# Performance work log

Hardware: AMD Instinct MI355X
Metric: run time of the kernel (lower is better)

The kernel has to match this reference:

```python
import jax, jax.numpy as jnp
import numpy as np

N_POINTS = 524288
N_VOXELS = 32768
C_IN = 6
GF = 64          # gf_dim
C_OUT = 256      # output_channels
HALF = C_OUT // 2


def _linear_params(key, fin, fout):
    kw, kb = jax.random.split(key)
    bound = 1.0 / np.sqrt(fin)
    W = jax.random.uniform(kw, (fin, fout), jnp.float32, -bound, bound)
    b = jax.random.uniform(kb, (fout,), jnp.float32, -bound, bound)
    return W, b


def setup_inputs() -> dict:
    key = jax.random.key(0)
    ks = jax.random.split(key, 8)
    inp_feat = jax.random.normal(ks[0], (N_POINTS, C_IN), dtype=jnp.float32)
    vox2point_idx = jax.random.randint(ks[1], (N_POINTS,), 0, N_VOXELS, dtype=jnp.int64)
    W1, b1 = _linear_params(ks[2], C_IN, GF)          # point_lin1
    W2, b2 = _linear_params(ks[3], GF, HALF)          # point_lin2
    Wv1, bv1 = _linear_params(ks[4], HALF, HALF)      # vox_lin1
    W3, b3 = _linear_params(ks[5], C_OUT, C_OUT)      # point_lin3
    W4, b4 = _linear_params(ks[6], C_OUT, C_OUT)      # point_lin4
    Wv2, bv2 = _linear_params(ks[7], C_OUT, C_OUT)    # vox_lin2
    return {
        "inp_feat": inp_feat, "vox2point_idx": vox2point_idx, "num_voxels": N_VOXELS,
        "W1": W1, "b1": b1, "W2": W2, "b2": b2, "Wv1": Wv1, "bv1": bv1,
        "W3": W3, "b3": b3, "W4": W4, "b4": b4, "Wv2": Wv2, "bv2": bv2,
    }


def reference(inp_feat, vox2point_idx, num_voxels,
              W1, b1, W2, b2, Wv1, bv1, W3, b3, W4, b4, Wv2, bv2):
    relu = jax.nn.relu
    # per-point MLP: [N,6] -> [N,64] -> [N,128]
    point_feat1 = relu(inp_feat @ W1 + b1)
    point_feat2 = relu(point_feat1 @ W2 + b2)
    # scatter-max pooling over voxels: [N,128] -> [V,128]
    occ_voxel_feat = jax.ops.segment_max(point_feat2, vox2point_idx,
                                         num_segments=num_voxels)
    occ_voxel_feat = relu(occ_voxel_feat @ Wv1 + bv1)
    # gather voxel feature back to points and concat: [N,128]+[N,128] -> [N,256]
    point_global_feat = occ_voxel_feat[vox2point_idx]
    point_feat3 = jnp.concatenate((point_global_feat, point_feat2), axis=-1)
    point_feat4 = relu(point_feat3 @ W3 + b3)
    point_feat5 = relu(point_feat4 @ W4 + b4)
    # second scatter-max pooling: [N,256] -> [V,256]
    occ_voxel_feat2 = jax.ops.segment_max(point_feat5, vox2point_idx,
                                          num_segments=num_voxels)
    occ_voxel_feat2 = relu(occ_voxel_feat2 @ Wv2 + bv2)
    return occ_voxel_feat2
```

## Files before the change

### kernel.cpp

```cpp
#include <hip/hip_runtime.h>


#define NPTS 524288
#define NVOX 32768

typedef _Float16 f16;
typedef _Float16 f16x8 __attribute__((ext_vector_type(8)));
typedef float f32x4 __attribute__((ext_vector_type(4)));

#define GLDS16(g, l)                                                          \
  __builtin_amdgcn_global_load_lds(                                           \
      (const __attribute__((address_space(1))) unsigned int*)(const void*)(g),\
      (__attribute__((address_space(3))) unsigned int*)(void*)(l), 16, 0, 0)

__global__ void k_fixidx(const int* __restrict__ raw, int* __restrict__ out) {
  bool is64 = true;
#pragma unroll
  for (int k = 0; k < 32; ++k)
    if (raw[2 * k + 1] != 0) is64 = false;
  int stride = gridDim.x * blockDim.x;
  for (int i = blockIdx.x * blockDim.x + threadIdx.x; i < NPTS; i += stride)
    out[i] = is64 ? raw[2 * i] : raw[i];
}

__global__ void k_hist(const int* __restrict__ idx, int* __restrict__ counts) {
  int stride = gridDim.x * blockDim.x;
  for (int i = blockIdx.x * blockDim.x + threadIdx.x; i < NPTS; i += stride)
    atomicAdd(&counts[idx[i]], 1);
}

__global__ void k_scan(const int* __restrict__ counts, int* __restrict__ offsets) {
  __shared__ int part[1024];
  __shared__ int sums[32];
  int t = threadIdx.x;
  int loc[32];
  int s = 0;
#pragma unroll
  for (int j = 0; j < 32; ++j) { loc[j] = counts[t * 32 + j]; s += loc[j]; }
  part[t] = s;
  __syncthreads();
  if (t < 32) {
    int run = 0;
    for (int j = 0; j < 32; ++j) { int tmp = part[t * 32 + j]; part[t * 32 + j] = run; run += tmp; }
    sums[t] = run;
  }
  __syncthreads();
  if (t == 0) {
    int run = 0;
    for (int i = 0; i < 32; ++i) { int tmp = sums[i]; sums[i] = run; run += tmp; }
  }
  __syncthreads();
  int b = part[t] + sums[t >> 5];
#pragma unroll
  for (int j = 0; j < 32; ++j) { offsets[t * 32 + j] = b; b += loc[j]; }
  if (t == 1023) offsets[NVOX] = b;
}

__global__ void k_scat(const int* __restrict__ idx, const int* __restrict__ offsets,
                       int* __restrict__ cursor, int* __restrict__ sp, int* __restrict__ sv) {
  int stride = gridDim.x * blockDim.x;
  for (int i = blockIdx.x * blockDim.x + threadIdx.x; i < NPTS; i += stride) {
    int v = idx[i];
    int pos = offsets[v] + atomicAdd(&cursor[v], 1);
    sp[pos] = i;
    sv[pos] = v;
  }
}

__global__ void k_wcast(const float* __restrict__ W, f16* __restrict__ Wt, int K, int N) {
  int g = blockIdx.x * blockDim.x + threadIdx.x;
  if (g >= K * N) return;
  int k = g / N, n = g % N;
  Wt[n * K + k] = (f16)W[g];
}

__global__ void k_castf(const float* __restrict__ in, f16* __restrict__ out, int n) {
  int stride = gridDim.x * blockDim.x;
  for (int i = blockIdx.x * blockDim.x + threadIdx.x; i < n; i += stride)
    out[i] = (f16)in[i];
}

template <int K, int N, int MODEA, bool SCATTER, bool OUTF32, bool WRITEO, bool WTILE>
__global__ __launch_bounds__(256, 3) void k_gemm(
    const f16* __restrict__ A,
    const int* __restrict__ sv, const int* __restrict__ sp,
    const int* __restrict__ offs,
    const float* __restrict__ x, const float* __restrict__ W1, const float* __restrict__ b1,
    const f16* __restrict__ Bt,
    const float* __restrict__ bias,
    f16* __restrict__ Of16, float* __restrict__ Of32, int row0) {
  constexpr int NT = N / 128;
  __shared__ __align__(16) char smem[32768];
  __shared__ float xs[MODEA == 2 ? 768 : 1];
  __shared__ int svp[MODEA == 2 ? 128 : 1];
  __shared__ int svx[SCATTER ? 128 : 1];
  f16* As = (f16*)smem;
  f16* Bs = As + 128 * 64;

  int nwg = gridDim.x;
  int bid = blockIdx.x;
  int q = nwg >> 3;
  int swz = (bid & 7) * q + (bid >> 3);
  int tm = swz / NT, tn = swz % NT;
  int t = threadIdx.x;

  if (MODEA == 2) { if (t < 128) svp[t] = sp[row0 + tm * 128 + t]; }
  if (SCATTER) { if (t < 128) svx[t] = sv[row0 + tm * 128 + t]; }
  if (MODEA == 2) __syncthreads();

  int l = t & 63, w = t >> 6;
  int wm = w >> 1, wn = w & 1;
  int lrow = l & 15, lk = l >> 4;
  f32x4 acc[4][4] = {};

  constexpr int KT = K / 64;
#pragma unroll
  for (int kt = 0; kt < KT; ++kt) {
    int k0 = kt * 64;
#pragma unroll
    for (int i = 0; i < 4; ++i) {
      int n = i * 32 + (t >> 3);
      int clog = (t & 7) ^ (n & 7);
      GLDS16(Bt + (size_t)(tn * 128 + n) * K + k0 + clog * 8, Bs + i * 2048 + t * 8);
    }
    if constexpr (MODEA == 2) {
      for (int g = t; g < 768; g += 256) xs[g] = x[(size_t)svp[g / 6] * 6 + (g % 6)];
      __syncthreads();
      int j = t & 63;
      float wv[6];
#pragma unroll
      for (int i = 0; i < 6; ++i) wv[i] = W1[i * 64 + j];
      float bb = b1[j];
      int rb = (t >> 6) * 32;
#pragma unroll
      for (int rr = 0; rr < 32; ++rr) {
        int row = rb + rr;
        float a = bb;
#pragma unroll
        for (int i = 0; i < 6; ++i) a += xs[row * 6 + i] * wv[i];
        As[row * 64 + (((j >> 3) ^ (row & 7)) << 3) + (j & 7)] = (f16)fmaxf(a, 0.f);
      }
    } else {
#pragma unroll
      for (int i = 0; i < 4; ++i) {
        int row = i * 32 + (t >> 3);
        int clog = (t & 7) ^ (row & 7);
        GLDS16(A + (size_t)(tm * 128 + row) * K + k0 + clog * 8, As + i * 2048 + t * 8);
      }
    }
    __syncthreads();
#pragma unroll
    for (int ks = 0; ks < 2; ++ks) {
      f16x8 af[4], bf[4];
#pragma unroll
      for (int m = 0; m < 4; ++m) {
        int row = wm * 64 + m * 16 + lrow;
        int cp = (ks * 4 + lk) ^ (row & 7);
        af[m] = *(const f16x8*)(As + row * 64 + cp * 8);
      }
#pragma unroll
      for (int n = 0; n < 4; ++n) {
        int col = wn * 64 + n * 16 + lrow;
        int cp = (ks * 4 + lk) ^ (col & 7);
        bf[n] = *(const f16x8*)(Bs + col * 64 + cp * 8);
      }
#pragma unroll
      for (int m = 0; m < 4; ++m)
#pragma unroll
        for (int n = 0; n < 4; ++n)
          acc[m][n] = __builtin_amdgcn_mfma_f32_16x16x32_f16(af[m], bf[n], acc[m][n], 0, 0, 0);
    }
    __syncthreads();
  }

  if constexpr (WRITEO) {
#pragma unroll
    for (int m = 0; m < 4; ++m)
#pragma unroll
      for (int n = 0; n < 4; ++n)
#pragma unroll
        for (int j = 0; j < 4; ++j) {
          int row = wm * 64 + m * 16 + lk * 4 + j;
          int gc  = tn * 128 + wn * 64 + n * 16 + lrow;
          float val = fmaxf(acc[m][n][j] + bias[gc], 0.f);
          if constexpr (OUTF32) Of32[(size_t)(tm * 128 + row) * N + gc] = val;
          else                  Of16[(size_t)(tm * 128 + row) * N + gc] = (f16)val;
        }
  }

  if constexpr (SCATTER) {
    f16* tile = (f16*)smem;
#pragma unroll
    for (int m = 0; m < 4; ++m)
#pragma unroll
      for (int n = 0; n < 4; ++n)
#pragma unroll
        for (int j = 0; j < 4; ++j) {
          int row = wm * 64 + m * 16 + lk * 4 + j;
          int col = wn * 64 + n * 16 + lrow;
          tile[row * 128 + col] =
              (f16)fmaxf(acc[m][n][j] + bias[tn * 128 + col], 0.f);
        }
    __syncthreads();
    if constexpr (WTILE) {
      f16* dst = Of16 + (size_t)(row0 + tm * 128) * 128;
#pragma unroll
      for (int i = 0; i < 8; ++i) {
        int g = i * 256 + t;
        *(f16x8*)(dst + g * 8) = *(const f16x8*)(tile + g * 8);
      }
    }
    int c = t & 127, h = t >> 7;
    int r0l = h * 64;
    int gc = tn * 128 + c;
    int grow0 = row0 + tm * 128 + r0l;
    float run = 0.f;
    int curv = svx[r0l];
    for (int r = r0l; r < r0l + 64; ++r) {
      int v = svx[r];
      if (v != curv) {
        bool inter = (offs[curv] >= grow0) && (offs[curv + 1] <= grow0 + 64);
        if (inter) Of32[(size_t)curv * N + gc] = run;
        else atomicMax((int*)&Of32[(size_t)curv * N + gc], __float_as_int(run));
        curv = v; run = 0.f;
      }
      run = fmaxf(run, (float)tile[r * 128 + c]);
    }
    bool inter = (offs[curv] >= grow0) && (offs[curv + 1] <= grow0 + 64);
    if (inter) Of32[(size_t)curv * N + gc] = run;
    else atomicMax((int*)&Of32[(size_t)curv * N + gc], __float_as_int(run));
  }
}

__global__ __launch_bounds__(512, 2) void k_stage2(
    const f16* __restrict__ pf2, const f16* __restrict__ occ1,
    const int* __restrict__ sv, const int* __restrict__ offs,
    const f16* __restrict__ W3t, const float* __restrict__ b3,
    const f16* __restrict__ W4t, const float* __restrict__ b4,
    float* __restrict__ vox2f, int row0) {
  __shared__ __align__(16) f16 Bs[256 * 32];
  __shared__ __align__(16) f16 PF[64 * 264];
  __shared__ int svx[64];

  int nwg = gridDim.x;
  int bid = blockIdx.x;
  int q = nwg >> 3;
  int bm = (bid & 7) * q + (bid >> 3);
  int t = threadIdx.x;
  int l = t & 63, w = t >> 6;
  int lrow = l & 15, lk = l >> 4;

  if (t < 64) svx[t] = sv[row0 + bm * 64 + t];
  __syncthreads();

  f16* Afull = PF;
#pragma unroll
  for (int ii = 0; ii < 4; ++ii) {
    int g = ii * 512 + t;
    int row = g >> 5, cs = g & 31;
    int cl = (cs & 24) | ((cs ^ row) & 7);
    const f16* src;
    if (cl < 16) src = occ1 + (size_t)svx[row] * 128 + cl * 8;
    else         src = pf2 + (size_t)(bm * 64 + row) * 128 + (cl - 16) * 8;
    GLDS16(src, Afull + g * 8);
  }
#pragma unroll
  for (int ii = 0; ii < 2; ++ii) {
    int g = ii * 512 + t;
    int n = g >> 2, c = g & 3;
    int cl = c ^ ((n >> 1) & 3);
    GLDS16(W3t + (size_t)n * 256 + cl * 8, Bs + g * 8);
  }
  __syncthreads();

  f32x4 acc[4][2] = {};

#pragma unroll
  for (int p = 0; p < 8; ++p) {
    f16x8 bf[2];
#pragma unroll
    for (int n = 0; n < 2; ++n) {
      int col = w * 32 + n * 16 + lrow;
      int cp = lk ^ ((col >> 1) & 3);
      bf[n] = *(const f16x8*)(Bs + col * 32 + cp * 8);
    }
    __syncthreads();
    {
      const f16* Wsrc = (p < 7) ? W3t : W4t;
      int kc = (p < 7) ? (p + 1) : 0;
#pragma unroll
      for (int ii = 0; ii < 2; ++ii) {
        int g = ii * 512 + t;
        int n = g >> 2, c = g & 3;
        int cl = c ^ ((n >> 1) & 3);
        GLDS16(Wsrc + (size_t)n * 256 + kc * 32 + cl * 8, Bs + g * 8);
      }
    }
    __builtin_amdgcn_s_setprio(1);
    f16x8 af[4];
#pragma unroll
    for (int m = 0; m < 4; ++m) {
      int row = m * 16 + lrow;
      int ab = p * 4 + lk;
      int slot = (ab & 24) | ((ab ^ row) & 7);
      af[m] = *(const f16x8*)(Afull + row * 256 + slot * 8);
    }
#pragma unroll
    for (int m = 0; m < 4; ++m)
#pragma unroll
      for (int n = 0; n < 2; ++n)
        acc[m][n] = __builtin_amdgcn_mfma_f32_16x16x32_f16(af[m], bf[n], acc[m][n], 0, 0, 0);
    __builtin_amdgcn_s_setprio(0);
    __syncthreads();
  }

  f16* pf4 = PF;
#pragma unroll
  for (int m = 0; m < 4; ++m)
#pragma unroll
    for (int n = 0; n < 2; ++n)
#pragma unroll
      for (int j = 0; j < 4; ++j) {
        int row  = m * 16 + lk * 4 + j;
        int colg = w * 32 + n * 16 + lrow;
        pf4[row * 264 + colg] = (f16)fmaxf(acc[m][n][j] + b3[colg], 0.f);
      }
  __syncthreads();

#pragma unroll
  for (int m = 0; m < 4; ++m)
#pragma unroll
    for (int n = 0; n < 2; ++n)
      acc[m][n] = (f32x4){0.f, 0.f, 0.f, 0.f};

#pragma unroll
  for (int p = 0; p < 8; ++p) {
    f16x8 bf[2];
#pragma unroll
    for (int n = 0; n < 2; ++n) {
      int col = w * 32 + n * 16 + lrow;
      int cp = lk ^ ((col >> 1) & 3);
      bf[n] = *(const f16x8*)(Bs + col * 32 + cp * 8);
    }
    __syncthreads();
    if (p < 7) {
#pragma unroll
      for (int ii = 0; ii < 2; ++ii) {
        int g = ii * 512 + t;
        int n = g >> 2, c = g & 3;
        int cl = c ^ ((n >> 1) & 3);
        GLDS16(W4t + (size_t)n * 256 + (p + 1) * 32 + cl * 8, Bs + g * 8);
      }
    }
    __builtin_amdgcn_s_setprio(1);
    f16x8 af[4];
#pragma unroll
    for (int m = 0; m < 4; ++m) {
      int row = m * 16 + lrow;
      int chunk = p * 4 + lk;
      af[m] = *(const f16x8*)(pf4 + row * 264 + chunk * 8);
    }
#pragma unroll
    for (int m = 0; m < 4; ++m)
#pragma unroll
      for (int n = 0; n < 2; ++n)
        acc[m][n] = __builtin_amdgcn_mfma_f32_16x16x32_f16(af[m], bf[n], acc[m][n], 0, 0, 0);
    __builtin_amdgcn_s_setprio(0);
    __syncthreads();
  }

  f16* pf5 = PF;
#pragma unroll
  for (int m = 0; m < 4; ++m)
#pragma unroll
    for (int n = 0; n < 2; ++n)
#pragma unroll
      for (int j = 0; j < 4; ++j) {
        int row  = m * 16 + lk * 4 + j;
        int colg = w * 32 + n * 16 + lrow;
        pf5[row * 264 + colg] = (f16)fmaxf(acc[m][n][j] + b4[colg], 0.f);
      }
  __syncthreads();

  {
    int c = t & 255, seg = t >> 8;
    int r0l = seg * 32;
    int grow0 = row0 + bm * 64 + r0l;
    float run = 0.f;
    int curv = svx[r0l];
    for (int r = r0l; r < r0l + 32; ++r) {
      int v = svx[r];
      if (v != curv) {
        bool inter = (offs[curv] >= grow0) && (offs[curv + 1] <= grow0 + 32);
        if (inter) vox2f[(size_t)curv * 256 + c] = run;
        else atomicMax((int*)&vox2f[(size_t)curv * 256 + c], __float_as_int(run));
        curv = v; run = 0.f;
      }
      run = fmaxf(run, (float)pf5[r * 264 + c]);
    }
    bool inter = (offs[curv] >= grow0) && (offs[curv + 1] <= grow0 + 32);
    if (inter) vox2f[(size_t)curv * 256 + c] = run;
    else atomicMax((int*)&vox2f[(size_t)curv * 256 + c], __float_as_int(run));
  }
}

extern "C" void kernel_launch(void* const* d_in, const int* in_sizes, int n_in,
                              void* d_out, int out_size, void* d_ws, size_t ws_size,
                              hipStream_t stream) {
  const float* x   = (const float*)d_in[0];
  const int*  idxr = (const int*)d_in[1];
  const float* W1  = (const float*)d_in[3];
  const float* b1  = (const float*)d_in[4];
  const float* W2  = (const float*)d_in[5];
  const float* b2  = (const float*)d_in[6];
  const float* Wv1 = (const float*)d_in[7];
  const float* bv1 = (const float*)d_in[8];
  const float* W3  = (const float*)d_in[9];
  const float* b3  = (const float*)d_in[10];
  const float* W4  = (const float*)d_in[11];
  const float* b4  = (const float*)d_in[12];
  const float* Wv2 = (const float*)d_in[13];
  const float* bv2 = (const float*)d_in[14];
  float* out = (float*)d_out;

  char* ws = (char*)d_ws;
  size_t off = 0;
  auto alloc = [&](size_t bytes) {
    void* p = ws + off;
    off = (off + bytes + 255) & ~(size_t)255;
    return p;
  };
  int* idx     = (int*)alloc((size_t)NPTS * 4);
  int* counts  = (int*)alloc((size_t)NVOX * 4);
  int* cursor  = (int*)alloc((size_t)NVOX * 4);
  int* offs    = (int*)alloc((size_t)(NVOX + 1) * 4);
  int* sp      = (int*)alloc((size_t)NPTS * 4);
  int* sv      = (int*)alloc((size_t)NPTS * 4);
  f16* W2t     = (f16*)alloc(64 * 128 * 2);
  f16* Wv1t    = (f16*)alloc(128 * 128 * 2);
  f16* W3t     = (f16*)alloc(256 * 256 * 2);
  f16* W4t     = (f16*)alloc(256 * 256 * 2);
  f16* Wv2t    = (f16*)alloc(256 * 256 * 2);
  float* vox1f = (float*)alloc((size_t)NVOX * 128 * 4);
  f16* vox1h   = (f16*)alloc((size_t)NVOX * 128 * 2);
  f16* occ1    = (f16*)alloc((size_t)NVOX * 128 * 2);
  float* vox2f = (float*)alloc((size_t)NVOX * 256 * 4);

  size_t rem = (ws_size > off) ? ws_size - off : 0;
  bool PF2FULL = rem >= (size_t)NPTS * 256 + 4096;
  int CH = 65536;
  f16* pf2   = (f16*)alloc(PF2FULL ? (size_t)NPTS * 256 : (size_t)CH * 256);
  f16* vox2h = pf2;

  hipMemsetAsync(counts, 0, (size_t)NVOX * 4, stream);
  hipMemsetAsync(cursor, 0, (size_t)NVOX * 4, stream);
  hipMemsetAsync(vox1f, 0, (size_t)NVOX * 128 * 4, stream);
  hipMemsetAsync(vox2f, 0, (size_t)NVOX * 256 * 4, stream);

  k_fixidx<<<2048, 256, 0, stream>>>(idxr, idx);
  k_wcast<<<(64 * 128 + 255) / 256, 256, 0, stream>>>(W2, W2t, 64, 128);
  k_wcast<<<(128 * 128 + 255) / 256, 256, 0, stream>>>(Wv1, Wv1t, 128, 128);
  k_wcast<<<(256 * 256 + 255) / 256, 256, 0, stream>>>(W3, W3t, 256, 256);
  k_wcast<<<(256 * 256 + 255) / 256, 256, 0, stream>>>(W4, W4t, 256, 256);
  k_wcast<<<(256 * 256 + 255) / 256, 256, 0, stream>>>(Wv2, Wv2t, 256, 256);
  k_hist<<<2048, 256, 0, stream>>>(idx, counts);
  k_scan<<<1, 1024, 0, stream>>>(counts, offs);
  k_scat<<<2048, 256, 0, stream>>>(idx, offs, cursor, sp, sv);

  if (PF2FULL)
    k_gemm<64, 128, 2, true, false, false, true><<<NPTS / 128, 256, 0, stream>>>(
        nullptr, sv, sp, offs, x, W1, b1, W2t, b2, pf2, vox1f, 0);
  else
    k_gemm<64, 128, 2, true, false, false, false><<<NPTS / 128, 256, 0, stream>>>(
        nullptr, sv, sp, offs, x, W1, b1, W2t, b2, nullptr, vox1f, 0);
  k_castf<<<2048, 256, 0, stream>>>(vox1f, vox1h, NVOX * 128);
  k_gemm<128, 128, 0, false, false, true, false><<<NVOX / 128, 256, 0, stream>>>(
      vox1h, nullptr, nullptr, nullptr, nullptr, nullptr, nullptr,
      Wv1t, bv1, occ1, nullptr, 0);

  if (PF2FULL) {
    k_stage2<<<NPTS / 64, 512, 0, stream>>>(
        pf2, occ1, sv, offs, W3t, b3, W4t, b4, vox2f, 0);
  } else {
    for (int c = 0; c < NPTS / CH; ++c) {
      int row0 = c * CH;
      k_gemm<64, 128, 2, false, false, true, false><<<CH / 128, 256, 0, stream>>>(
          nullptr, nullptr, sp, nullptr, x, W1, b1, W2t, b2, pf2, nullptr, row0);
      k_stage2<<<CH / 64, 512, 0, stream>>>(
          pf2, occ1, sv, offs, W3t, b3, W4t, b4, vox2f, row0);
    }
  }

  k_castf<<<2048, 256, 0, stream>>>(vox2f, vox2h, NVOX * 256);
  k_gemm<256, 256, 0, false, true, true, false><<<(NVOX / 128) * 2, 256, 0, stream>>>(
      vox2h, nullptr, nullptr, nullptr, nullptr, nullptr, nullptr,
      Wv2t, bv2, nullptr, out, 0);
}
```

Before: 387.0 us.

## Precompute voxel half of point_lin3 per voxel instead of per point

Splits W3 into a voxel half and a point half. The voxel half (occ1 @ W3top + b3) is computed once per voxel by a new GEMM into a voxc buffer. k_stage2 then gathers that precomputed partial sum into its accumulators and runs only the K=128 point half. This removes half of the per-point layer-3 matmul FLOPs. In exchange it adds a small extra GEMM, a 32768x256 f16 intermediate, scalar per-element gathers of voxc into registers, and XOR swizzling of the pf4/pf5 LDS tiles.

```diff
diff --git a/kernel.cpp b/kernel.cpp
--- a/kernel.cpp
+++ b/kernel.cpp
@@ -74,13 +74,20 @@
   Wt[n * K + k] = (f16)W[g];
 }
 
+__global__ void k_wcast2(const float* __restrict__ W, f16* __restrict__ Wt, int k0) {
+  int g = blockIdx.x * blockDim.x + threadIdx.x;
+  if (g >= 256 * 128) return;
+  int n = g >> 7, k = g & 127;
+  Wt[g] = (f16)W[(size_t)(k0 + k) * 256 + n];
+}
+
 __global__ void k_castf(const float* __restrict__ in, f16* __restrict__ out, int n) {
   int stride = gridDim.x * blockDim.x;
   for (int i = blockIdx.x * blockDim.x + threadIdx.x; i < n; i += stride)
     out[i] = (f16)in[i];
 }
 
-template <int K, int N, int MODEA, bool SCATTER, bool OUTF32, bool WRITEO, bool WTILE>
+template <int K, int N, int MODEA, bool SCATTER, bool OUTF32, bool WRITEO, bool WTILE, bool RELU>
 __global__ __launch_bounds__(256, 3) void k_gemm(
     const f16* __restrict__ A,
     const int* __restrict__ sv, const int* __restrict__ sp,
@@ -182,7 +189,8 @@
         for (int j = 0; j < 4; ++j) {
           int row = wm * 64 + m * 16 + lk * 4 + j;
           int gc  = tn * 128 + wn * 64 + n * 16 + lrow;
-          float val = fmaxf(acc[m][n][j] + bias[gc], 0.f);
+          float val = acc[m][n][j] + bias[gc];
+          if constexpr (RELU) val = fmaxf(val, 0.f);
           if constexpr (OUTF32) Of32[(size_t)(tm * 128 + row) * N + gc] = val;
           else                  Of16[(size_t)(tm * 128 + row) * N + gc] = (f16)val;
         }
@@ -233,14 +241,18 @@
 }
 
 __global__ __launch_bounds__(512, 2) void k_stage2(
-    const f16* __restrict__ pf2, const f16* __restrict__ occ1,
+    const f16* __restrict__ pf2, const f16* __restrict__ voxc,
     const int* __restrict__ sv, const int* __restrict__ offs,
-    const f16* __restrict__ W3t, const float* __restrict__ b3,
-    const f16* __restrict__ W4t, const float* __restrict__ b4,
+    const f16* __restrict__ W3bt,
+    const f16* __restrict__ W4t,
+    const float* __restrict__ b4,
     float* __restrict__ vox2f, int row0) {
-  __shared__ __align__(16) f16 Bs[256 * 32];
-  __shared__ __align__(16) f16 PF[64 * 264];
+  __shared__ __align__(16) char smem[49152];
   __shared__ int svx[64];
+  f16* As  = (f16*)smem;
+  f16* Bs  = (f16*)(smem + 32768);
+  f16* pf4 = (f16*)smem;
+  f16* pf5 = pf4;
 
   int nwg = gridDim.x;
   int bid = blockIdx.x;
@@ -253,30 +265,34 @@
   if (t < 64) svx[t] = sv[row0 + bm * 64 + t];
   __syncthreads();
 
-  f16* Afull = PF;
-#pragma unroll
-  for (int ii = 0; ii < 4; ++ii) {
+#pragma unroll
+  for (int ii = 0; ii < 2; ++ii) {
     int g = ii * 512 + t;
-    int row = g >> 5, cs = g & 31;
-    int cl = (cs & 24) | ((cs ^ row) & 7);
-    const f16* src;
-    if (cl < 16) src = occ1 + (size_t)svx[row] * 128 + cl * 8;
-    else         src = pf2 + (size_t)(bm * 64 + row) * 128 + (cl - 16) * 8;
-    GLDS16(src, Afull + g * 8);
+    int row = g >> 4, cs = g & 15;
+    int cl = (cs & 8) | ((cs ^ row) & 7);
+    GLDS16(pf2 + (size_t)(bm * 64 + row) * 128 + cl * 8, As + g * 8);
   }
 #pragma unroll
   for (int ii = 0; ii < 2; ++ii) {
     int g = ii * 512 + t;
     int n = g >> 2, c = g & 3;
     int cl = c ^ ((n >> 1) & 3);
-    GLDS16(W3t + (size_t)n * 256 + cl * 8, Bs + g * 8);
-  }
-  __syncthreads();
-
-  f32x4 acc[4][2] = {};
-
-#pragma unroll
-  for (int p = 0; p < 8; ++p) {
+    GLDS16(W3bt + (size_t)n * 128 + cl * 8, Bs + g * 8);
+  }
+  f32x4 acc[4][2];
+#pragma unroll
+  for (int m = 0; m < 4; ++m)
+#pragma unroll
+    for (int j = 0; j < 4; ++j) {
+      int v = svx[m * 16 + lk * 4 + j];
+#pragma unroll
+      for (int n = 0; n < 2; ++n)
+        acc[m][n][j] = (float)voxc[(size_t)v * 256 + w * 32 + n * 16 + lrow];
+    }
+  __syncthreads();
+
+#pragma unroll
+  for (int p = 0; p < 4; ++p) {
     f16x8 bf[2];
 #pragma unroll
     for (int n = 0; n < 2; ++n) {
@@ -285,15 +301,21 @@
       bf[n] = *(const f16x8*)(Bs + col * 32 + cp * 8);
     }
     __syncthreads();
-    {
-      const f16* Wsrc = (p < 7) ? W3t : W4t;
-      int kc = (p < 7) ? (p + 1) : 0;
+    if (p < 3) {
 #pragma unroll
       for (int ii = 0; ii < 2; ++ii) {
         int g = ii * 512 + t;
         int n = g >> 2, c = g & 3;
         int cl = c ^ ((n >> 1) & 3);
-        GLDS16(Wsrc + (size_t)n * 256 + kc * 32 + cl * 8, Bs + g * 8);
+        GLDS16(W3bt + (size_t)n * 128 + (p + 1) * 32 + cl * 8, Bs + g * 8);
+      }
+    } else {
+#pragma unroll
+      for (int ii = 0; ii < 2; ++ii) {
+        int g = ii * 512 + t;
+        int n = g >> 2, c = g & 3;
+        int cl = c ^ ((n >> 1) & 3);
+        GLDS16(W4t + (size_t)n * 256 + cl * 8, Bs + g * 8);
       }
     }
     __builtin_amdgcn_s_setprio(1);
@@ -302,8 +324,8 @@
     for (int m = 0; m < 4; ++m) {
       int row = m * 16 + lrow;
       int ab = p * 4 + lk;
-      int slot = (ab & 24) | ((ab ^ row) & 7);
-      af[m] = *(const f16x8*)(Afull + row * 256 + slot * 8);
+      int slot = (ab & 8) | ((ab ^ row) & 7);
+      af[m] = *(const f16x8*)(As + row * 128 + slot * 8);
     }
 #pragma unroll
     for (int m = 0; m < 4; ++m)
@@ -314,7 +336,6 @@
     __syncthreads();
   }
 
-  f16* pf4 = PF;
 #pragma unroll
   for (int m = 0; m < 4; ++m)
 #pragma unroll
@@ -323,7 +344,9 @@
       for (int j = 0; j < 4; ++j) {
         int row  = m * 16 + lk * 4 + j;
         int colg = w * 32 + n * 16 + lrow;
-        pf4[row * 264 + colg] = (f16)fmaxf(acc[m][n][j] + b3[colg], 0.f);
+        int ch = colg >> 3;
+        int sc = (ch & 24) | ((ch ^ row) & 7);
+        pf4[row * 256 + sc * 8 + (colg & 7)] = (f16)fmaxf(acc[m][n][j], 0.f);
       }
   __syncthreads();
 
@@ -358,7 +381,8 @@
     for (int m = 0; m < 4; ++m) {
       int row = m * 16 + lrow;
       int chunk = p * 4 + lk;
-      af[m] = *(const f16x8*)(pf4 + row * 264 + chunk * 8);
+      int slot = (chunk & 24) | ((chunk ^ row) & 7);
+      af[m] = *(const f16x8*)(pf4 + row * 256 + slot * 8);
     }
 #pragma unroll
     for (int m = 0; m < 4; ++m)
@@ -369,7 +393,6 @@
     __syncthreads();
   }
 
-  f16* pf5 = PF;
 #pragma unroll
   for (int m = 0; m < 4; ++m)
 #pragma unroll
@@ -378,7 +401,9 @@
       for (int j = 0; j < 4; ++j) {
         int row  = m * 16 + lk * 4 + j;
         int colg = w * 32 + n * 16 + lrow;
-        pf5[row * 264 + colg] = (f16)fmaxf(acc[m][n][j] + b4[colg], 0.f);
+        int ch = colg >> 3;
+        int sc = (ch & 24) | ((ch ^ row) & 7);
+        pf5[row * 256 + sc * 8 + (colg & 7)] = (f16)fmaxf(acc[m][n][j] + b4[colg], 0.f);
       }
   __syncthreads();
 
@@ -388,6 +413,7 @@
     int grow0 = row0 + bm * 64 + r0l;
     float run = 0.f;
     int curv = svx[r0l];
+    int ch = c >> 3;
     for (int r = r0l; r < r0l + 32; ++r) {
       int v = svx[r];
       if (v != curv) {
@@ -396,7 +422,8 @@
         else atomicMax((int*)&vox2f[(size_t)curv * 256 + c], __float_as_int(run));
         curv = v; run = 0.f;
       }
-      run = fmaxf(run, (float)pf5[r * 264 + c]);
+      int sc = (ch & 24) | ((ch ^ r) & 7);
+      run = fmaxf(run, (float)pf5[r * 256 + sc * 8 + (c & 7)]);
     }
     bool inter = (offs[curv] >= grow0) && (offs[curv + 1] <= grow0 + 32);
     if (inter) vox2f[(size_t)curv * 256 + c] = run;
@@ -438,12 +465,14 @@
   int* sv      = (int*)alloc((size_t)NPTS * 4);
   f16* W2t     = (f16*)alloc(64 * 128 * 2);
   f16* Wv1t    = (f16*)alloc(128 * 128 * 2);
-  f16* W3t     = (f16*)alloc(256 * 256 * 2);
+  f16* W3topt  = (f16*)alloc(256 * 128 * 2);
+  f16* W3bott  = (f16*)alloc(256 * 128 * 2);
   f16* W4t     = (f16*)alloc(256 * 256 * 2);
   f16* Wv2t    = (f16*)alloc(256 * 256 * 2);
   float* vox1f = (float*)alloc((size_t)NVOX * 128 * 4);
   f16* vox1h   = (f16*)alloc((size_t)NVOX * 128 * 2);
   f16* occ1    = (f16*)alloc((size_t)NVOX * 128 * 2);
+  f16* voxc    = (f16*)alloc((size_t)NVOX * 256 * 2);
   float* vox2f = (float*)alloc((size_t)NVOX * 256 * 4);
 
   size_t rem = (ws_size > off) ? ws_size - off : 0;
@@ -460,7 +489,8 @@
   k_fixidx<<<2048, 256, 0, stream>>>(idxr, idx);
   k_wcast<<<(64 * 128 + 255) / 256, 256, 0, stream>>>(W2, W2t, 64, 128);
   k_wcast<<<(128 * 128 + 255) / 256, 256, 0, stream>>>(Wv1, Wv1t, 128, 128);
-  k_wcast<<<(256 * 256 + 255) / 256, 256, 0, stream>>>(W3, W3t, 256, 256);
+  k_wcast2<<<(256 * 128 + 255) / 256, 256, 0, stream>>>(W3, W3topt, 0);
+  k_wcast2<<<(256 * 128 + 255) / 256, 256, 0, stream>>>(W3, W3bott, 128);
   k_wcast<<<(256 * 256 + 255) / 256, 256, 0, stream>>>(W4, W4t, 256, 256);
   k_wcast<<<(256 * 256 + 255) / 256, 256, 0, stream>>>(Wv2, Wv2t, 256, 256);
   k_hist<<<2048, 256, 0, stream>>>(idx, counts);
@@ -468,31 +498,34 @@
   k_scat<<<2048, 256, 0, stream>>>(idx, offs, cursor, sp, sv);
 
   if (PF2FULL)
-    k_gemm<64, 128, 2, true, false, false, true><<<NPTS / 128, 256, 0, stream>>>(
+    k_gemm<64, 128, 2, true, false, false, true, true><<<NPTS / 128, 256, 0, stream>>>(
         nullptr, sv, sp, offs, x, W1, b1, W2t, b2, pf2, vox1f, 0);
   else
-    k_gemm<64, 128, 2, true, false, false, false><<<NPTS / 128, 256, 0, stream>>>(
+    k_gemm<64, 128, 2, true, false, false, false, true><<<NPTS / 128, 256, 0, stream>>>(
         nullptr, sv, sp, offs, x, W1, b1, W2t, b2, nullptr, vox1f, 0);
   k_castf<<<2048, 256, 0, stream>>>(vox1f, vox1h, NVOX * 128);
-  k_gemm<128, 128, 0, false, false, true, false><<<NVOX / 128, 256, 0, stream>>>(
+  k_gemm<128, 128, 0, false, false, true, false, true><<<NVOX / 128, 256, 0, stream>>>(
       vox1h, nullptr, nullptr, nullptr, nullptr, nullptr, nullptr,
       Wv1t, bv1, occ1, nullptr, 0);
+  k_gemm<128, 256, 0, false, false, true, false, false><<<(NVOX / 128) * 2, 256, 0, stream>>>(
+      occ1, nullptr, nullptr, nullptr, nullptr, nullptr, nullptr,
+      W3topt, b3, voxc, nullptr, 0);
 
   if (PF2FULL) {
     k_stage2<<<NPTS / 64, 512, 0, stream>>>(
-        pf2, occ1, sv, offs, W3t, b3, W4t, b4, vox2f, 0);
+        pf2, voxc, sv, offs, W3bott, W4t, b4, vox2f, 0);
   } else {
     for (int c = 0; c < NPTS / CH; ++c) {
       int row0 = c * CH;
-      k_gemm<64, 128, 2, false, false, true, false><<<CH / 128, 256, 0, stream>>>(
+      k_gemm<64, 128, 2, false, false, true, false, true><<<CH / 128, 256, 0, stream>>>(
           nullptr, nullptr, sp, nullptr, x, W1, b1, W2t, b2, pf2, nullptr, row0);
       k_stage2<<<CH / 64, 512, 0, stream>>>(
-          pf2, occ1, sv, offs, W3t, b3, W4t, b4, vox2f, row0);
+          pf2, voxc, sv, offs, W3bott, W4t, b4, vox2f, row0);
     }
   }
 
   k_castf<<<2048, 256, 0, stream>>>(vox2f, vox2h, NVOX * 256);
-  k_gemm<256, 256, 0, false, true, true, false><<<(NVOX / 128) * 2, 256, 0, stream>>>(
+  k_gemm<256, 256, 0, false, true, true, false, true><<<(NVOX / 128) * 2, 256, 0, stream>>>(
       vox2h, nullptr, nullptr, nullptr, nullptr, nullptr, nullptr,
       Wv2t, bv2, nullptr, out, 0);
 }
```

Result: slower. 430.7 us (+11.3%).

## Split first MLP layer into standalone kernel and XOR-swizzle stage2 LDS tile

Applied to the files above, without the earlier changes.

Adds a k_mlp1 kernel that computes the 6->64 layer in sorted point order and writes an f16 intermediate buffer. When workspace allows, the first GEMM then reads it in MODEA 0 instead of recomputing the layer inline. Separately, the stage2 shared tile drops its 264-element row padding in favour of an XOR swizzle on 8-element chunks, which shrinks LDS use while aiming to keep reads conflict-free. The split costs an extra NPTS*64 f16 write and read through global memory plus one more launch.

```diff
diff --git a/kernel.cpp b/kernel.cpp
--- a/kernel.cpp
+++ b/kernel.cpp
@@ -64,6 +64,39 @@
     int pos = offsets[v] + atomicAdd(&cursor[v], 1);
     sp[pos] = i;
     sv[pos] = v;
+  }
+}
+
+__global__ void k_mlp1(const float* __restrict__ x, const int* __restrict__ sp,
+                       const float* __restrict__ W1, const float* __restrict__ b1,
+                       f16* __restrict__ pf1) {
+  __shared__ float w[384];
+  __shared__ float bb[64];
+  int t = threadIdx.x;
+  if (t < 384) w[t] = W1[t];
+  if (t < 64) bb[t] = b1[t];
+  __syncthreads();
+  int stride = gridDim.x * blockDim.x;
+  for (int s = blockIdx.x * blockDim.x + t; s < NPTS; s += stride) {
+    int p = sp[s];
+    const float* src = x + (size_t)p * 6;
+    float x0 = src[0], x1 = src[1], x2 = src[2];
+    float x3 = src[3], x4 = src[4], x5 = src[5];
+    f16* dst = pf1 + (size_t)s * 64;
+#pragma unroll
+    for (int j0 = 0; j0 < 64; j0 += 8) {
+      f16x8 o;
+#pragma unroll
+      for (int u = 0; u < 8; ++u) {
+        int j = j0 + u;
+        float a = bb[j];
+        a += x0 * w[j];       a += x1 * w[64 + j];
+        a += x2 * w[128 + j]; a += x3 * w[192 + j];
+        a += x4 * w[256 + j]; a += x5 * w[320 + j];
+        o[u] = (f16)fmaxf(a, 0.f);
+      }
+      *(f16x8*)(dst + j0) = o;
+    }
   }
 }
 
@@ -239,7 +272,7 @@
     const f16* __restrict__ W4t, const float* __restrict__ b4,
     float* __restrict__ vox2f, int row0) {
   __shared__ __align__(16) f16 Bs[256 * 32];
-  __shared__ __align__(16) f16 PF[64 * 264];
+  __shared__ __align__(16) f16 PF[64 * 256];
   __shared__ int svx[64];
 
   int nwg = gridDim.x;
@@ -323,7 +356,9 @@
       for (int j = 0; j < 4; ++j) {
         int row  = m * 16 + lk * 4 + j;
         int colg = w * 32 + n * 16 + lrow;
-        pf4[row * 264 + colg] = (f16)fmaxf(acc[m][n][j] + b3[colg], 0.f);
+        int ch = colg >> 3;
+        int sc = (ch & 24) | ((ch ^ row) & 7);
+        pf4[row * 256 + sc * 8 + (colg & 7)] = (f16)fmaxf(acc[m][n][j] + b3[colg], 0.f);
       }
   __syncthreads();
 
@@ -358,7 +393,8 @@
     for (int m = 0; m < 4; ++m) {
       int row = m * 16 + lrow;
       int chunk = p * 4 + lk;
-      af[m] = *(const f16x8*)(pf4 + row * 264 + chunk * 8);
+      int slot = (chunk & 24) | ((chunk ^ row) & 7);
+      af[m] = *(const f16x8*)(pf4 + row * 256 + slot * 8);
     }
 #pragma unroll
     for (int m = 0; m < 4; ++m)
@@ -378,7 +414,9 @@
       for (int j = 0; j < 4; ++j) {
         int row  = m * 16 + lk * 4 + j;
         int colg = w * 32 + n * 16 + lrow;
-        pf5[row * 264 + colg] = (f16)fmaxf(acc[m][n][j] + b4[colg], 0.f);
+        int ch = colg >> 3;
+        int sc = (ch & 24) | ((ch ^ row) & 7);
+        pf5[row * 256 + sc * 8 + (colg & 7)] = (f16)fmaxf(acc[m][n][j] + b4[colg], 0.f);
       }
   __syncthreads();
 
@@ -388,6 +426,7 @@
     int grow0 = row0 + bm * 64 + r0l;
     float run = 0.f;
     int curv = svx[r0l];
+    int ch = c >> 3;
     for (int r = r0l; r < r0l + 32; ++r) {
       int v = svx[r];
       if (v != curv) {
@@ -396,7 +435,8 @@
         else atomicMax((int*)&vox2f[(size_t)curv * 256 + c], __float_as_int(run));
         curv = v; run = 0.f;
       }
-      run = fmaxf(run, (float)pf5[r * 264 + c]);
+      int sc = (ch & 24) | ((ch ^ r) & 7);
+      run = fmaxf(run, (float)pf5[r * 256 + sc * 8 + (c & 7)]);
     }
     bool inter = (offs[curv] >= grow0) && (offs[curv + 1] <= grow0 + 32);
     if (inter) vox2f[(size_t)curv * 256 + c] = run;
@@ -451,6 +491,9 @@
   int CH = 65536;
   f16* pf2   = (f16*)alloc(PF2FULL ? (size_t)NPTS * 256 : (size_t)CH * 256);
   f16* vox2h = pf2;
+  size_t rem2 = (ws_size > off) ? ws_size - off : 0;
+  bool MLP1SPLIT = PF2FULL && rem2 >= (size_t)NPTS * 128 + 4096;
+  f16* pf1 = MLP1SPLIT ? (f16*)alloc((size_t)NPTS * 128) : nullptr;
 
   hipMemsetAsync(counts, 0, (size_t)NVOX * 4, stream);
   hipMemsetAsync(cursor, 0, (size_t)NVOX * 4, stream);
@@ -467,12 +510,17 @@
   k_scan<<<1, 1024, 0, stream>>>(counts, offs);
   k_scat<<<2048, 256, 0, stream>>>(idx, offs, cursor, sp, sv);
 
-  if (PF2FULL)
+  if (MLP1SPLIT) {
+    k_mlp1<<<2048, 256, 0, stream>>>(x, sp, W1, b1, pf1);
+    k_gemm<64, 128, 0, true, false, false, true><<<NPTS / 128, 256, 0, stream>>>(
+        pf1, sv, sp, offs, x, W1, b1, W2t, b2, pf2, vox1f, 0);
+  } else if (PF2FULL) {
     k_gemm<64, 128, 2, true, false, false, true><<<NPTS / 128, 256, 0, stream>>>(
         nullptr, sv, sp, offs, x, W1, b1, W2t, b2, pf2, vox1f, 0);
-  else
+  } else {
     k_gemm<64, 128, 2, true, false, false, false><<<NPTS / 128, 256, 0, stream>>>(
         nullptr, sv, sp, offs, x, W1, b1, W2t, b2, nullptr, vox1f, 0);
+  }
   k_castf<<<2048, 256, 0, stream>>>(vox1f, vox1h, NVOX * 128);
   k_gemm<128, 128, 0, false, false, true, false><<<NVOX / 128, 256, 0, stream>>>(
       vox1h, nullptr, nullptr, nullptr, nullptr, nullptr, nullptr,
```

Result: slower. 420.9 us (+8.8%).
